# Performance work log

Measured on AMD Instinct MI355X. Metric: run time of the kernel, lower is better.

## Reference

```python
import jax, jax.numpy as jnp
import numpy as np

B, S, C, H = 2, 4096, 640, 8
D = C // H  # head_dim = 80


def setup_inputs() -> dict:
    key = jax.random.key(0)
    ks = jax.random.split(key, 5)
    init = 0.02
    return {
        "hidden_states": jax.random.normal(ks[0], (B, S, C), dtype=jnp.float32),
        "Wq": jax.random.normal(ks[1], (C, C), dtype=jnp.float32) * init,
        "Wk": jax.random.normal(ks[2], (C, C), dtype=jnp.float32) * init,
        "Wv": jax.random.normal(ks[3], (C, C), dtype=jnp.float32) * init,
        "Wo": jax.random.normal(ks[4], (C, C), dtype=jnp.float32) * init,
        "bo": jnp.zeros((C,), dtype=jnp.float32),
    }


def reference(hidden_states, Wq, Wk, Wv, Wo, bo):
    # self-attention: encoder_hidden_states is None -> k,v from hidden_states
    x = hidden_states  # [B, S, C]
    q = jnp.einsum("bsc,cd->bsd", x, Wq)
    k = jnp.einsum("bsc,cd->bsd", x, Wk)
    v = jnp.einsum("bsc,cd->bsd", x, Wv)

    # head_to_batch_dim: [B, S, H*D] -> [B, H, S, D]
    def split_heads(t):
        return t.reshape(B, S, H, D).transpose(0, 2, 1, 3)

    q, k, v = split_heads(q), split_heads(k), split_heads(v)

    scale = 1.0 / jnp.sqrt(jnp.float32(D))
    # get_attention_scores: baddbmm(q, k^T) * scale, softmax over keys
    scores = jnp.einsum("bhqd,bhkd->bhqk", q, k) * scale  # [B, H, S, S]
    probs = jax.nn.softmax(scores, axis=-1)
    out = jnp.einsum("bhqk,bhkd->bhqd", probs, v)  # [B, H, S, D]

    # batch_to_head_dim + to_out[0] linear (Dropout is identity at eval)
    out = out.transpose(0, 2, 1, 3).reshape(B, S, C)
    out = jnp.einsum("bsc,cd->bsd", out, Wo) + bo
    # residual_connection=False, rescale_output_factor=1.0 (diffusers defaults)
    return out
```

## Files before the change

kernel.cpp:

```cpp
#include <hip/hip_runtime.h>
#include <hip/hip_bf16.h>

typedef __bf16 bf16x8 __attribute__((ext_vector_type(8)));
typedef float f32x4 __attribute__((ext_vector_type(4)));
typedef float f32x16 __attribute__((ext_vector_type(16)));
typedef unsigned short u16;
typedef unsigned int u32;
typedef u16 u16x8 __attribute__((ext_vector_type(8)));

#define DEV __device__ __forceinline__

DEV u16 f2b(float f) {
    u32 u = __builtin_bit_cast(u32, f);
    u32 r = (u + 0x7FFFu + ((u >> 16) & 1u)) >> 16;
    return (u16)r;
}
DEV bf16x8 load8(const u16* p) {
    return __builtin_bit_cast(bf16x8, *(const uint4*)p);
}
DEV u32 cvtpk(float lo, float hi) {
    u32 r;
    asm("v_cvt_pk_bf16_f32 %0, %1, %2" : "=v"(r) : "v"(lo), "v"(hi));
    return r;
}
DEV void gld_lds16(const u16* g, const char* l) {
    __builtin_amdgcn_global_load_lds(
        (const __attribute__((address_space(1))) u32*)(unsigned long long)g,
        (__attribute__((address_space(3))) u32*)(u32)(unsigned long long)l,
        16, 0, 0);
}

__global__ __launch_bounds__(256) void cvt_x(const float* __restrict__ X, u16* __restrict__ Xb) {
    long i = ((long)blockIdx.x * 256 + threadIdx.x) * 8;
    float fa[8];
    *(uint4*)fa = *(const uint4*)(X + i);
    *(uint4*)(fa + 4) = *(const uint4*)(X + i + 4);
    u16x8 t;
    #pragma unroll
    for (int j = 0; j < 8; ++j) t[j] = f2b(fa[j]);
    *(u16x8*)(Xb + i) = t;
}

__global__ __launch_bounds__(256) void cvt_w4(
    const float* __restrict__ Wq, const float* __restrict__ Wk,
    const float* __restrict__ Wv, const float* __restrict__ Wo,
    u16* __restrict__ Wt4)
{
    const int z = blockIdx.z;
    const float* W = (z == 0) ? Wq : ((z == 1) ? Wk : ((z == 2) ? Wv : Wo));
    u16* Wt = Wt4 + (long)z * 409600;
    const int k0 = blockIdx.x * 64, n0 = blockIdx.y * 64;
    const int t = threadIdx.x;
    __shared__ u16 T[64][72];
    {
        int kl = t >> 2, nc = (t & 3) * 16;
        const float* src = W + (long)(k0 + kl) * 640 + n0 + nc;
        float fa[16];
        #pragma unroll
        for (int i = 0; i < 4; ++i) *(uint4*)(fa + i * 4) = *(const uint4*)(src + i * 4);
        #pragma unroll
        for (int j = 0; j < 16; ++j) T[nc + j][kl] = f2b(fa[j]);
    }
    __syncthreads();
    {
        int nl = t >> 2, kc = (t & 3) * 16;
        u16* dst = Wt + (long)(n0 + nl) * 640 + k0 + kc;
        *(uint4*)dst = *(const uint4*)&T[nl][kc];
        *(uint4*)(dst + 8) = *(const uint4*)&T[nl][kc + 8];
    }
}

#define GEMM_CORE(A_PTR, BT_PTR)                                                  \
    const int tid = threadIdx.x;                                                  \
    const int lane = tid & 63;                                                    \
    const int w = tid >> 6;                                                       \
    const int wm = w >> 1, wn = w & 1;                                            \
    const int lg = lane >> 4, lr = lane & 15;                                     \
    __shared__ __align__(16) char Bb[2][16384];                                   \
    auto stage = [&](int kt0, int buf) {                                          \
        _Pragma("unroll")                                                         \
        for (int i = 0; i < 4; ++i) {                                             \
            int c = i * 256 + tid;                                                \
            int n = c >> 3, cc = c & 7;                                           \
            gld_lds16(BT_PTR + (long)(n0 + n) * 640 + kt0 + ((cc ^ (n & 7)) * 8), \
                      Bb[buf] + (c & ~63) * 16);                                  \
        }                                                                         \
    };                                                                            \
    f32x4 acc[4][4] = {};                                                         \
    stage(0, 0);                                                                  \
    for (int t = 0; t < 10; ++t) {                                                \
        __syncthreads();                                                          \
        if (t < 9) stage((t + 1) * 64, (t + 1) & 1);                              \
        const char* Bc = Bb[t & 1];                                               \
        _Pragma("unroll")                                                         \
        for (int ks = 0; ks < 64; ks += 32) {                                     \
            bf16x8 a[4], b[4];                                                    \
            _Pragma("unroll")                                                     \
            for (int mi = 0; mi < 4; ++mi) {                                      \
                int row = m0 + wm * 64 + mi * 16 + lr;                            \
                a[mi] = load8(A_PTR + (long)row * 640 + t * 64 + ks + lg * 8);    \
            }                                                                     \
            _Pragma("unroll")                                                     \
            for (int ni = 0; ni < 4; ++ni) {                                      \
                int n = wn * 64 + ni * 16 + lr;                                   \
                int cc = (ks >> 3) + lg;                                          \
                b[ni] = __builtin_bit_cast(bf16x8,                                \
                    *(const uint4*)(Bc + (n * 8 + (cc ^ (n & 7))) * 16));         \
            }                                                                     \
            _Pragma("unroll")                                                     \
            for (int mi = 0; mi < 4; ++mi)                                        \
                _Pragma("unroll")                                                 \
                for (int ni = 0; ni < 4; ++ni)                                    \
                    acc[mi][ni] = __builtin_amdgcn_mfma_f32_16x16x32_bf16(        \
                        a[mi], b[ni], acc[mi][ni], 0, 0, 0);                      \
        }                                                                         \
    }

__global__ __launch_bounds__(256, 3) void gemm_qkv(
    const u16* __restrict__ X, const u16* __restrict__ Wt3,
    u16* __restrict__ q_ws, u16* __restrict__ k_ws, u16* __restrict__ v_ws)
{
    const int z = blockIdx.z;
    const u16* Wt = Wt3 + (long)z * 409600;
    const int m0 = blockIdx.x * 128;
    const int n0 = blockIdx.y * 128;
    GEMM_CORE(X, Wt)
    #pragma unroll
    for (int mi = 0; mi < 4; ++mi)
        #pragma unroll
        for (int ni = 0; ni < 4; ++ni)
            #pragma unroll
            for (int r = 0; r < 4; ++r) {
                int m = m0 + wm * 64 + mi * 16 + lg * 4 + r;
                int n = n0 + wn * 64 + ni * 16 + lr;
                int b_ = m >> 12, s = m & 4095;
                int h = n / 80, d = n % 80;
                long bh = b_ * 8 + h;
                int tt = s >> 6, jj = s & 63;
                float val = acc[mi][ni][r];
                if (z == 0) {
                    q_ws[(bh * 4096 + s) * 80 + d] = f2b(val * 0.16131517891624225f);
                } else if (z == 1) {
                    k_ws[(bh * 64 + tt) * 5120 + (((d >> 4) * 2 + ((d >> 3) & 1)) * 64 + jj) * 8 + (d & 7)] = f2b(val);
                } else {
                    int kb = jj >> 5, h2 = (jj >> 4) & 1, hv = (jj >> 2) & 1;
                    int jv = ((jj >> 3) & 1) * 4 + (jj & 3);
                    int c = kb * 2 + h2;
                    u16* vt = v_ws + (bh * 64 + tt) * 6144;
                    vt[((c * 2 + hv) * 96 + d) * 8 + jv] = f2b(val);
                    if (d == 0) vt[((c * 2 + hv) * 96 + 80) * 8 + jv] = 0x3F80;
                }
            }
}

__global__ __launch_bounds__(256, 3) void gemm_out(
    const u16* __restrict__ X, const u16* __restrict__ Wt,
    const float* __restrict__ bias, float* __restrict__ out)
{
    const int m0 = blockIdx.x * 128;
    const int n0 = blockIdx.y * 128;
    GEMM_CORE(X, Wt)
    #pragma unroll
    for (int mi = 0; mi < 4; ++mi)
        #pragma unroll
        for (int ni = 0; ni < 4; ++ni)
            #pragma unroll
            for (int r = 0; r < 4; ++r) {
                int m = m0 + wm * 64 + mi * 16 + lg * 4 + r;
                int n = n0 + wn * 64 + ni * 16 + lr;
                out[(long)m * 640 + n] = acc[mi][ni][r] + bias[n];
            }
}

__global__ __launch_bounds__(256, 2) void attn(
    const u16* __restrict__ q_ws, const u16* __restrict__ k_ws,
    const u16* __restrict__ v_ws, u16* __restrict__ o_ws)
{
    const int l = blockIdx.x;
    const int xcd = l & 7, inner = l >> 3;
    const int bh = (xcd << 1) | (inner >> 5);
    const int qx = inner & 31;
    const int qb = qx * 128;
    const int tid = threadIdx.x;
    const int lane = tid & 63;
    const int w = tid >> 6;
    const int hi = lane >> 5;
    const int lq = lane & 31;

    __shared__ __align__(16) char Kb[2][10240];
    __shared__ __align__(16) char Vb[2][12288];

    const u16* ktile = k_ws + (long)bh * 64 * 5120;
    const u16* vtile = v_ws + (long)bh * 64 * 6144;

    bf16x8 qf[5];
    const int qrow = qb + w * 32 + lq;
    #pragma unroll
    for (int kc = 0; kc < 5; ++kc)
        qf[kc] = load8(q_ws + ((long)bh * 4096 + qrow) * 80 + kc * 16 + hi * 8);

    f32x16 acc[3] = {};

    auto stage = [&](int t, int buf) {
        const u16* kt_ = ktile + (long)t * 5120;
        const u16* vt_ = vtile + (long)t * 6144;
        #pragma unroll
        for (int i = 0; i < 6; ++i) {
            int c = i * 256 + tid;
            if (c < 1408) {
                int cw = c & ~63;
                if (cw < 640) gld_lds16(kt_ + (long)c * 8, Kb[buf] + cw * 16);
                else          gld_lds16(vt_ + (long)(c - 640) * 8, Vb[buf] + (cw - 640) * 16);
            }
        }
    };

    stage(0, 0);
    for (int t = 0; t < 64; ++t) {
        __syncthreads();
        if (t < 63) stage(t + 1, (t + 1) & 1);
        const char* Kc = Kb[t & 1];
        const char* Vc = Vb[t & 1];

        f32x16 sf[2] = {};
        __builtin_amdgcn_s_setprio(1);
        #pragma unroll
        for (int kc = 0; kc < 5; ++kc) {
            #pragma unroll
            for (int kb = 0; kb < 2; ++kb) {
                bf16x8 kf = __builtin_bit_cast(bf16x8,
                    *(const uint4*)(Kc + ((kc * 2 + hi) * 64 + kb * 32 + lq) * 16));
                sf[kb] = __builtin_amdgcn_mfma_f32_32x32x16_bf16(kf, qf[kc], sf[kb], 0, 0, 0);
            }
        }
        __builtin_amdgcn_s_setprio(0);

        #pragma unroll
        for (int kb = 0; kb < 2; ++kb)
            #pragma unroll
            for (int r = 0; r < 16; ++r)
                sf[kb][r] = __builtin_amdgcn_exp2f(sf[kb][r]);

        bf16x8 pa[4];
        #pragma unroll
        for (int kb = 0; kb < 2; ++kb)
            #pragma unroll
            for (int h = 0; h < 2; ++h) {
                uint4 wv;
                wv.x = cvtpk(sf[kb][h * 8 + 0], sf[kb][h * 8 + 1]);
                wv.y = cvtpk(sf[kb][h * 8 + 2], sf[kb][h * 8 + 3]);
                wv.z = cvtpk(sf[kb][h * 8 + 4], sf[kb][h * 8 + 5]);
                wv.w = cvtpk(sf[kb][h * 8 + 6], sf[kb][h * 8 + 7]);
                pa[kb * 2 + h] = __builtin_bit_cast(bf16x8, wv);
            }

        __builtin_amdgcn_s_setprio(1);
        #pragma unroll
        for (int db = 0; db < 3; ++db)
            #pragma unroll
            for (int c = 0; c < 4; ++c) {
                bf16x8 vf = __builtin_bit_cast(bf16x8,
                    *(const uint4*)(Vc + ((c * 2 + hi) * 96 + db * 32 + lq) * 16));
                acc[db] = __builtin_amdgcn_mfma_f32_32x32x16_bf16(pa[c], vf, acc[db], 0, 0, 0);
            }
        __builtin_amdgcn_s_setprio(0);
    }

    const int b_ = bh >> 3, h8 = bh & 7;
    #pragma unroll
    for (int r = 0; r < 16; ++r) {
        int ql = (r & 3) + 8 * (r >> 2) + 4 * hi;
        float lsum = __shfl(acc[2][r], (hi << 5) + 16);
        float inv = 1.0f / lsum;
        int row = qb + w * 32 + ql;
        #pragma unroll
        for (int db = 0; db < 3; ++db) {
            int d = db * 32 + lq;
            if (d < 80)
                o_ws[((long)b_ * 4096 + row) * 640 + h8 * 80 + d] = f2b(acc[db][r] * inv);
        }
    }
}

extern "C" void kernel_launch(void* const* d_in, const int* in_sizes, int n_in,
                              void* d_out, int out_size, void* d_ws, size_t ws_size,
                              hipStream_t stream) {
    const float* x  = (const float*)d_in[0];
    const float* Wq = (const float*)d_in[1];
    const float* Wk = (const float*)d_in[2];
    const float* Wv = (const float*)d_in[3];
    const float* Wo = (const float*)d_in[4];
    const float* bo = (const float*)d_in[5];

    u16* ws = (u16*)d_ws;
    const long SZ = 5242880;
    u16* Xb   = ws;
    u16* q_ws = ws + SZ;
    u16* k_ws = ws + 2 * SZ;
    u16* v_ws = ws + 3 * SZ;
    u16* Wt4  = ws + 3 * SZ + 6291456;
    u16* o_ws = Xb;
    u16* WtO  = Wt4 + 3 * 409600;

    cvt_x<<<2560, 256, 0, stream>>>(x, Xb);
    dim3 gw4(10, 10, 4);
    cvt_w4<<<gw4, 256, 0, stream>>>(Wq, Wk, Wv, Wo, Wt4);

    dim3 g1(64, 5, 3);
    gemm_qkv<<<g1, 256, 0, stream>>>(Xb, Wt4, q_ws, k_ws, v_ws);

    attn<<<512, 256, 0, stream>>>(q_ws, k_ws, v_ws, o_ws);

    dim3 g3(64, 5);
    gemm_out<<<g3, 256, 0, stream>>>(o_ws, WtO, bo, (float*)d_out);
}
```

Measured before the change: 196.5 us.

## Software-pipeline attention QK with softmax/PV and merge conversion kernels

The attention loop is restructured so the QK^T MFMAs for the next key tile are issued before the exp/convert/PV work of the current tile, with V triple-buffered and K double-buffered in LDS. This is meant to overlap the exponential and conversion VALU work with matrix instructions and hide load latency. The two fp32-to-bf16 conversion kernels are also merged into one launch to save launch overhead. In exchange LDS use and register pressure go up, which could reduce occupancy. The clamped staging at the loop tail also issues redundant loads.

```diff
diff --git a/kernel.cpp b/kernel.cpp
--- a/kernel.cpp
+++ b/kernel.cpp
@@ -30,26 +30,30 @@
         16, 0, 0);
 }
 
-__global__ __launch_bounds__(256) void cvt_x(const float* __restrict__ X, u16* __restrict__ Xb) {
-    long i = ((long)blockIdx.x * 256 + threadIdx.x) * 8;
-    float fa[8];
-    *(uint4*)fa = *(const uint4*)(X + i);
-    *(uint4*)(fa + 4) = *(const uint4*)(X + i + 4);
-    u16x8 t;
-    #pragma unroll
-    for (int j = 0; j < 8; ++j) t[j] = f2b(fa[j]);
-    *(u16x8*)(Xb + i) = t;
-}
-
-__global__ __launch_bounds__(256) void cvt_w4(
+__global__ __launch_bounds__(256) void cvt_all(
+    const float* __restrict__ X, u16* __restrict__ Xb,
     const float* __restrict__ Wq, const float* __restrict__ Wk,
     const float* __restrict__ Wv, const float* __restrict__ Wo,
     u16* __restrict__ Wt4)
 {
-    const int z = blockIdx.z;
+    const int bx = blockIdx.x;
+    if (bx < 2560) {
+        long i = ((long)bx * 256 + threadIdx.x) * 8;
+        float fa[8];
+        *(uint4*)fa = *(const uint4*)(X + i);
+        *(uint4*)(fa + 4) = *(const uint4*)(X + i + 4);
+        u16x8 t;
+        #pragma unroll
+        for (int j = 0; j < 8; ++j) t[j] = f2b(fa[j]);
+        *(u16x8*)(Xb + i) = t;
+        return;
+    }
+    const int idx = bx - 2560;
+    const int z = idx / 100;
+    const int rem = idx % 100;
+    const int k0 = (rem / 10) * 64, n0 = (rem % 10) * 64;
     const float* W = (z == 0) ? Wq : ((z == 1) ? Wk : ((z == 2) ? Wv : Wo));
     u16* Wt = Wt4 + (long)z * 409600;
-    const int k0 = blockIdx.x * 64, n0 = blockIdx.y * 64;
     const int t = threadIdx.x;
     __shared__ u16 T[64][72];
     {
@@ -188,7 +192,7 @@
     const int lq = lane & 31;
 
     __shared__ __align__(16) char Kb[2][10240];
-    __shared__ __align__(16) char Vb[2][12288];
+    __shared__ __align__(16) char Vb[3][12288];
 
     const u16* ktile = k_ws + (long)bh * 64 * 5120;
     const u16* vtile = v_ws + (long)bh * 64 * 6144;
@@ -201,28 +205,26 @@
 
     f32x16 acc[3] = {};
 
-    auto stage = [&](int t, int buf) {
+    auto stageK = [&](int t, int buf) {
         const u16* kt_ = ktile + (long)t * 5120;
+        #pragma unroll
+        for (int i = 0; i < 3; ++i) {
+            int c = i * 256 + tid;
+            if (c < 640) gld_lds16(kt_ + (long)c * 8, Kb[buf] + (c & ~63) * 16);
+        }
+    };
+    auto stageV = [&](int t, int buf) {
         const u16* vt_ = vtile + (long)t * 6144;
         #pragma unroll
-        for (int i = 0; i < 6; ++i) {
+        for (int i = 0; i < 3; ++i) {
             int c = i * 256 + tid;
-            if (c < 1408) {
-                int cw = c & ~63;
-                if (cw < 640) gld_lds16(kt_ + (long)c * 8, Kb[buf] + cw * 16);
-                else          gld_lds16(vt_ + (long)(c - 640) * 8, Vb[buf] + (cw - 640) * 16);
-            }
+            gld_lds16(vt_ + (long)c * 8, Vb[buf] + (c & ~63) * 16);
         }
     };
-
-    stage(0, 0);
-    for (int t = 0; t < 64; ++t) {
-        __syncthreads();
-        if (t < 63) stage(t + 1, (t + 1) & 1);
-        const char* Kc = Kb[t & 1];
-        const char* Vc = Vb[t & 1];
-
-        f32x16 sf[2] = {};
+    auto QK = [&](int kbuf, f32x16* sf) {
+        const char* Kc = Kb[kbuf];
+        f32x16 z = {};
+        sf[0] = z; sf[1] = z;
         __builtin_amdgcn_s_setprio(1);
         #pragma unroll
         for (int kc = 0; kc < 5; ++kc) {
@@ -234,13 +236,14 @@
             }
         }
         __builtin_amdgcn_s_setprio(0);
-
+    };
+    auto SM_PV = [&](f32x16* sf, int vbuf) {
+        const char* Vc = Vb[vbuf];
         #pragma unroll
         for (int kb = 0; kb < 2; ++kb)
             #pragma unroll
             for (int r = 0; r < 16; ++r)
                 sf[kb][r] = __builtin_amdgcn_exp2f(sf[kb][r]);
-
         bf16x8 pa[4];
         #pragma unroll
         for (int kb = 0; kb < 2; ++kb)
@@ -253,7 +256,6 @@
                 wv.w = cvtpk(sf[kb][h * 8 + 6], sf[kb][h * 8 + 7]);
                 pa[kb * 2 + h] = __builtin_bit_cast(bf16x8, wv);
             }
-
         __builtin_amdgcn_s_setprio(1);
         #pragma unroll
         for (int db = 0; db < 3; ++db)
@@ -264,6 +266,31 @@
                 acc[db] = __builtin_amdgcn_mfma_f32_32x32x16_bf16(pa[c], vf, acc[db], 0, 0, 0);
             }
         __builtin_amdgcn_s_setprio(0);
+    };
+
+    f32x16 sfA[2], sfB[2];
+    stageK(0, 0); stageV(0, 0);
+    __syncthreads();
+    stageK(1, 1); stageV(1, 1);
+    QK(0, sfA);
+
+    for (int t = 0; t < 64; t += 2) {
+        __syncthreads();
+        {
+            int ts = (t + 2 < 64) ? t + 2 : 63;
+            stageK(ts, t & 1);
+            stageV(ts, (t + 2) % 3);
+        }
+        QK((t + 1) & 1, sfB);
+        SM_PV(sfA, t % 3);
+        __syncthreads();
+        {
+            int ts = (t + 3 < 64) ? t + 3 : 63;
+            stageK(ts, (t + 1) & 1);
+            stageV(ts, (t + 3) % 3);
+        }
+        QK(t & 1, sfA);
+        SM_PV(sfB, (t + 1) % 3);
     }
 
     const int b_ = bh >> 3, h8 = bh & 7;
@@ -302,9 +329,7 @@
     u16* o_ws = Xb;
     u16* WtO  = Wt4 + 3 * 409600;
 
-    cvt_x<<<2560, 256, 0, stream>>>(x, Xb);
-    dim3 gw4(10, 10, 4);
-    cvt_w4<<<gw4, 256, 0, stream>>>(Wq, Wk, Wv, Wo, Wt4);
+    cvt_all<<<2960, 256, 0, stream>>>(x, Xb, Wq, Wk, Wv, Wo, Wt4);
 
     dim3 g1(64, 5, 3);
     gemm_qkv<<<g1, 256, 0, stream>>>(Xb, Wt4, q_ws, k_ws, v_ws);
```

Measured after the change: 192.4 us. 2.1% less time.

## Split attention key tiles across wave pairs and merge conversion kernels

Applied to the files above, without the earlier changes.

The attention kernel now uses 64-row query blocks. Each pair of waves shares one 32-row query slice and splits every 64-key tile in half, so twice as many workgroups launch and occupancy hints go from 2 to 3 blocks per CU. At the end the partial output accumulators (row sums included) are added through shared memory, which costs an extra reduction, more K/V tile loads per query row, and more LDS use. Separately, the X and weight conversion kernels are fused into a single launch to drop one kernel launch.

```diff
diff --git a/kernel.cpp b/kernel.cpp
--- a/kernel.cpp
+++ b/kernel.cpp
@@ -30,26 +30,30 @@
         16, 0, 0);
 }
 
-__global__ __launch_bounds__(256) void cvt_x(const float* __restrict__ X, u16* __restrict__ Xb) {
-    long i = ((long)blockIdx.x * 256 + threadIdx.x) * 8;
-    float fa[8];
-    *(uint4*)fa = *(const uint4*)(X + i);
-    *(uint4*)(fa + 4) = *(const uint4*)(X + i + 4);
-    u16x8 t;
-    #pragma unroll
-    for (int j = 0; j < 8; ++j) t[j] = f2b(fa[j]);
-    *(u16x8*)(Xb + i) = t;
-}
-
-__global__ __launch_bounds__(256) void cvt_w4(
+__global__ __launch_bounds__(256) void cvt_all(
+    const float* __restrict__ X, u16* __restrict__ Xb,
     const float* __restrict__ Wq, const float* __restrict__ Wk,
     const float* __restrict__ Wv, const float* __restrict__ Wo,
     u16* __restrict__ Wt4)
 {
-    const int z = blockIdx.z;
+    const int bx = blockIdx.x;
+    if (bx < 2560) {
+        long i = ((long)bx * 256 + threadIdx.x) * 8;
+        float fa[8];
+        *(uint4*)fa = *(const uint4*)(X + i);
+        *(uint4*)(fa + 4) = *(const uint4*)(X + i + 4);
+        u16x8 t;
+        #pragma unroll
+        for (int j = 0; j < 8; ++j) t[j] = f2b(fa[j]);
+        *(u16x8*)(Xb + i) = t;
+        return;
+    }
+    const int idx = bx - 2560;
+    const int z = idx / 100;
+    const int rem = idx % 100;
+    const int k0 = (rem / 10) * 64, n0 = (rem % 10) * 64;
     const float* W = (z == 0) ? Wq : ((z == 1) ? Wk : ((z == 2) ? Wv : Wo));
     u16* Wt = Wt4 + (long)z * 409600;
-    const int k0 = blockIdx.x * 64, n0 = blockIdx.y * 64;
     const int t = threadIdx.x;
     __shared__ u16 T[64][72];
     {
@@ -172,29 +176,32 @@
             }
 }
 
-__global__ __launch_bounds__(256, 2) void attn(
+__global__ __launch_bounds__(256, 3) void attn(
     const u16* __restrict__ q_ws, const u16* __restrict__ k_ws,
     const u16* __restrict__ v_ws, u16* __restrict__ o_ws)
 {
     const int l = blockIdx.x;
     const int xcd = l & 7, inner = l >> 3;
-    const int bh = (xcd << 1) | (inner >> 5);
-    const int qx = inner & 31;
-    const int qb = qx * 128;
+    const int bh = (xcd << 1) | (inner >> 6);
+    const int qx = inner & 63;
+    const int qb = qx * 64;
     const int tid = threadIdx.x;
     const int lane = tid & 63;
     const int w = tid >> 6;
+    const int wq = w >> 1;
+    const int kb = w & 1;
     const int hi = lane >> 5;
     const int lq = lane & 31;
 
-    __shared__ __align__(16) char Kb[2][10240];
-    __shared__ __align__(16) char Vb[2][12288];
+    __shared__ __align__(16) char S[45056];
+    char* Kb = S;
+    char* Vb = S + 20480;
 
     const u16* ktile = k_ws + (long)bh * 64 * 5120;
     const u16* vtile = v_ws + (long)bh * 64 * 6144;
 
     bf16x8 qf[5];
-    const int qrow = qb + w * 32 + lq;
+    const int qrow = qb + wq * 32 + lq;
     #pragma unroll
     for (int kc = 0; kc < 5; ++kc)
         qf[kc] = load8(q_ws + ((long)bh * 4096 + qrow) * 80 + kc * 16 + hi * 8);
@@ -209,8 +216,8 @@
             int c = i * 256 + tid;
             if (c < 1408) {
                 int cw = c & ~63;
-                if (cw < 640) gld_lds16(kt_ + (long)c * 8, Kb[buf] + cw * 16);
-                else          gld_lds16(vt_ + (long)(c - 640) * 8, Vb[buf] + (cw - 640) * 16);
+                if (cw < 640) gld_lds16(kt_ + (long)c * 8, Kb + buf * 10240 + cw * 16);
+                else          gld_lds16(vt_ + (long)(c - 640) * 8, Vb + buf * 12288 + (cw - 640) * 16);
             }
         }
     };
@@ -219,65 +226,84 @@
     for (int t = 0; t < 64; ++t) {
         __syncthreads();
         if (t < 63) stage(t + 1, (t + 1) & 1);
-        const char* Kc = Kb[t & 1];
-        const char* Vc = Vb[t & 1];
-
-        f32x16 sf[2] = {};
+        const char* Kc = Kb + (t & 1) * 10240;
+        const char* Vc = Vb + (t & 1) * 12288;
+
+        f32x16 sf = {};
         __builtin_amdgcn_s_setprio(1);
         #pragma unroll
         for (int kc = 0; kc < 5; ++kc) {
-            #pragma unroll
-            for (int kb = 0; kb < 2; ++kb) {
-                bf16x8 kf = __builtin_bit_cast(bf16x8,
-                    *(const uint4*)(Kc + ((kc * 2 + hi) * 64 + kb * 32 + lq) * 16));
-                sf[kb] = __builtin_amdgcn_mfma_f32_32x32x16_bf16(kf, qf[kc], sf[kb], 0, 0, 0);
-            }
+            bf16x8 kf = __builtin_bit_cast(bf16x8,
+                *(const uint4*)(Kc + ((kc * 2 + hi) * 64 + kb * 32 + lq) * 16));
+            sf = __builtin_amdgcn_mfma_f32_32x32x16_bf16(kf, qf[kc], sf, 0, 0, 0);
         }
         __builtin_amdgcn_s_setprio(0);
 
         #pragma unroll
-        for (int kb = 0; kb < 2; ++kb)
-            #pragma unroll
-            for (int r = 0; r < 16; ++r)
-                sf[kb][r] = __builtin_amdgcn_exp2f(sf[kb][r]);
-
-        bf16x8 pa[4];
-        #pragma unroll
-        for (int kb = 0; kb < 2; ++kb)
+        for (int r = 0; r < 16; ++r)
+            sf[r] = __builtin_amdgcn_exp2f(sf[r]);
+
+        bf16x8 pa[2];
+        #pragma unroll
+        for (int h = 0; h < 2; ++h) {
+            uint4 wv;
+            wv.x = cvtpk(sf[h * 8 + 0], sf[h * 8 + 1]);
+            wv.y = cvtpk(sf[h * 8 + 2], sf[h * 8 + 3]);
+            wv.z = cvtpk(sf[h * 8 + 4], sf[h * 8 + 5]);
+            wv.w = cvtpk(sf[h * 8 + 6], sf[h * 8 + 7]);
+            pa[h] = __builtin_bit_cast(bf16x8, wv);
+        }
+
+        __builtin_amdgcn_s_setprio(1);
+        #pragma unroll
+        for (int db = 0; db < 3; ++db)
             #pragma unroll
             for (int h = 0; h < 2; ++h) {
-                uint4 wv;
-                wv.x = cvtpk(sf[kb][h * 8 + 0], sf[kb][h * 8 + 1]);
-                wv.y = cvtpk(sf[kb][h * 8 + 2], sf[kb][h * 8 + 3]);
-                wv.z = cvtpk(sf[kb][h * 8 + 4], sf[kb][h * 8 + 5]);
-                wv.w = cvtpk(sf[kb][h * 8 + 6], sf[kb][h * 8 + 7]);
-                pa[kb * 2 + h] = __builtin_bit_cast(bf16x8, wv);
-            }
-
-        __builtin_amdgcn_s_setprio(1);
+                bf16x8 vf = __builtin_bit_cast(bf16x8,
+                    *(const uint4*)(Vc + (((kb * 2 + h) * 2 + hi) * 96 + db * 32 + lq) * 16));
+                acc[db] = __builtin_amdgcn_mfma_f32_32x32x16_bf16(pa[h], vf, acc[db], 0, 0, 0);
+            }
+        __builtin_amdgcn_s_setprio(0);
+    }
+
+    __syncthreads();
+    float* comb = (float*)S;
+    const int crow = wq * 64 + lane;
+    if (kb == 1) {
         #pragma unroll
         for (int db = 0; db < 3; ++db)
             #pragma unroll
-            for (int c = 0; c < 4; ++c) {
-                bf16x8 vf = __builtin_bit_cast(bf16x8,
-                    *(const uint4*)(Vc + ((c * 2 + hi) * 96 + db * 32 + lq) * 16));
-                acc[db] = __builtin_amdgcn_mfma_f32_32x32x16_bf16(pa[c], vf, acc[db], 0, 0, 0);
-            }
-        __builtin_amdgcn_s_setprio(0);
-    }
-
-    const int b_ = bh >> 3, h8 = bh & 7;
-    #pragma unroll
-    for (int r = 0; r < 16; ++r) {
-        int ql = (r & 3) + 8 * (r >> 2) + 4 * hi;
-        float lsum = __shfl(acc[2][r], (hi << 5) + 16);
-        float inv = 1.0f / lsum;
-        int row = qb + w * 32 + ql;
-        #pragma unroll
-        for (int db = 0; db < 3; ++db) {
-            int d = db * 32 + lq;
-            if (d < 80)
-                o_ws[((long)b_ * 4096 + row) * 640 + h8 * 80 + d] = f2b(acc[db][r] * inv);
+            for (int j = 0; j < 4; ++j) {
+                f32x4 v4 = { acc[db][j * 4 + 0], acc[db][j * 4 + 1],
+                             acc[db][j * 4 + 2], acc[db][j * 4 + 3] };
+                *(f32x4*)(comb + crow * 48 + db * 16 + j * 4) = v4;
+            }
+    }
+    __syncthreads();
+    if (kb == 0) {
+        #pragma unroll
+        for (int db = 0; db < 3; ++db)
+            #pragma unroll
+            for (int j = 0; j < 4; ++j) {
+                f32x4 v4 = *(const f32x4*)(comb + crow * 48 + db * 16 + j * 4);
+                acc[db][j * 4 + 0] += v4[0];
+                acc[db][j * 4 + 1] += v4[1];
+                acc[db][j * 4 + 2] += v4[2];
+                acc[db][j * 4 + 3] += v4[3];
+            }
+        const int b_ = bh >> 3, h8 = bh & 7;
+        #pragma unroll
+        for (int r = 0; r < 16; ++r) {
+            int ql = (r & 3) + 8 * (r >> 2) + 4 * hi;
+            float lsum = __shfl(acc[2][r], (hi << 5) + 16);
+            float inv = 1.0f / lsum;
+            int row = qb + wq * 32 + ql;
+            #pragma unroll
+            for (int db = 0; db < 3; ++db) {
+                int d = db * 32 + lq;
+                if (d < 80)
+                    o_ws[((long)b_ * 4096 + row) * 640 + h8 * 80 + d] = f2b(acc[db][r] * inv);
+            }
         }
     }
 }
@@ -302,14 +328,12 @@
     u16* o_ws = Xb;
     u16* WtO  = Wt4 + 3 * 409600;
 
-    cvt_x<<<2560, 256, 0, stream>>>(x, Xb);
-    dim3 gw4(10, 10, 4);
-    cvt_w4<<<gw4, 256, 0, stream>>>(Wq, Wk, Wv, Wo, Wt4);
+    cvt_all<<<2960, 256, 0, stream>>>(x, Xb, Wq, Wk, Wv, Wo, Wt4);
 
     dim3 g1(64, 5, 3);
     gemm_qkv<<<g1, 256, 0, stream>>>(Xb, Wt4, q_ws, k_ws, v_ws);
 
-    attn<<<512, 256, 0, stream>>>(q_ws, k_ws, v_ws, o_ws);
+    attn<<<1024, 256, 0, stream>>>(q_ws, k_ws, v_ws, o_ws);
 
     dim3 g3(64, 5);
     gemm_out<<<g3, 256, 0, stream>>>(o_ws, WtO, bo, (float*)d_out);
```

Measured after the change: 219.8 us. 11.9% more time.

## Double query rows per wave in attention and merge conversion kernels

Applied to the files above, without the earlier changes.

Each attention wave now handles 64 query rows, split into two 32-row halves that share every K and V fragment read from LDS. This halves the grid to 256 blocks and drops the occupancy hint to 1 block per CU. The aim is to halve LDS fragment reads and global K/V staging per query row. The cost is roughly double the accumulator register pressure and fewer resident waves to hide latency. Separately, the X and weight conversion kernels are merged into one launch to save a kernel launch.

```diff
diff --git a/kernel.cpp b/kernel.cpp
--- a/kernel.cpp
+++ b/kernel.cpp
@@ -30,26 +30,30 @@
         16, 0, 0);
 }
 
-__global__ __launch_bounds__(256) void cvt_x(const float* __restrict__ X, u16* __restrict__ Xb) {
-    long i = ((long)blockIdx.x * 256 + threadIdx.x) * 8;
-    float fa[8];
-    *(uint4*)fa = *(const uint4*)(X + i);
-    *(uint4*)(fa + 4) = *(const uint4*)(X + i + 4);
-    u16x8 t;
-    #pragma unroll
-    for (int j = 0; j < 8; ++j) t[j] = f2b(fa[j]);
-    *(u16x8*)(Xb + i) = t;
-}
-
-__global__ __launch_bounds__(256) void cvt_w4(
+__global__ __launch_bounds__(256) void cvt_all(
+    const float* __restrict__ X, u16* __restrict__ Xb,
     const float* __restrict__ Wq, const float* __restrict__ Wk,
     const float* __restrict__ Wv, const float* __restrict__ Wo,
     u16* __restrict__ Wt4)
 {
-    const int z = blockIdx.z;
+    const int bx = blockIdx.x;
+    if (bx < 2560) {
+        long i = ((long)bx * 256 + threadIdx.x) * 8;
+        float fa[8];
+        *(uint4*)fa = *(const uint4*)(X + i);
+        *(uint4*)(fa + 4) = *(const uint4*)(X + i + 4);
+        u16x8 t;
+        #pragma unroll
+        for (int j = 0; j < 8; ++j) t[j] = f2b(fa[j]);
+        *(u16x8*)(Xb + i) = t;
+        return;
+    }
+    const int idx = bx - 2560;
+    const int z = idx / 100;
+    const int rem = idx % 100;
+    const int k0 = (rem / 10) * 64, n0 = (rem % 10) * 64;
     const float* W = (z == 0) ? Wq : ((z == 1) ? Wk : ((z == 2) ? Wv : Wo));
     u16* Wt = Wt4 + (long)z * 409600;
-    const int k0 = blockIdx.x * 64, n0 = blockIdx.y * 64;
     const int t = threadIdx.x;
     __shared__ u16 T[64][72];
     {
@@ -172,15 +176,15 @@
             }
 }
 
-__global__ __launch_bounds__(256, 2) void attn(
+__global__ __launch_bounds__(256, 1) void attn(
     const u16* __restrict__ q_ws, const u16* __restrict__ k_ws,
     const u16* __restrict__ v_ws, u16* __restrict__ o_ws)
 {
     const int l = blockIdx.x;
     const int xcd = l & 7, inner = l >> 3;
-    const int bh = (xcd << 1) | (inner >> 5);
-    const int qx = inner & 31;
-    const int qb = qx * 128;
+    const int bh = (xcd << 1) | (inner >> 4);
+    const int qx = inner & 15;
+    const int qb = qx * 256;
     const int tid = threadIdx.x;
     const int lane = tid & 63;
     const int w = tid >> 6;
@@ -193,13 +197,15 @@
     const u16* ktile = k_ws + (long)bh * 64 * 5120;
     const u16* vtile = v_ws + (long)bh * 64 * 6144;
 
-    bf16x8 qf[5];
-    const int qrow = qb + w * 32 + lq;
+    bf16x8 qfA[5], qfB[5];
+    const long qbase = ((long)bh * 4096 + qb + w * 64 + lq) * 80;
     #pragma unroll
-    for (int kc = 0; kc < 5; ++kc)
-        qf[kc] = load8(q_ws + ((long)bh * 4096 + qrow) * 80 + kc * 16 + hi * 8);
-
-    f32x16 acc[3] = {};
+    for (int kc = 0; kc < 5; ++kc) {
+        qfA[kc] = load8(q_ws + qbase + kc * 16 + hi * 8);
+        qfB[kc] = load8(q_ws + qbase + 32 * 80 + kc * 16 + hi * 8);
+    }
+
+    f32x16 accA[3] = {}, accB[3] = {};
 
     auto stage = [&](int t, int buf) {
         const u16* kt_ = ktile + (long)t * 5120;
@@ -222,37 +228,54 @@
         const char* Kc = Kb[t & 1];
         const char* Vc = Vb[t & 1];
 
-        f32x16 sf[2] = {};
+        f32x16 sfA0 = {}, sfA1 = {}, sfB0 = {}, sfB1 = {};
         __builtin_amdgcn_s_setprio(1);
         #pragma unroll
         for (int kc = 0; kc < 5; ++kc) {
-            #pragma unroll
-            for (int kb = 0; kb < 2; ++kb) {
-                bf16x8 kf = __builtin_bit_cast(bf16x8,
-                    *(const uint4*)(Kc + ((kc * 2 + hi) * 64 + kb * 32 + lq) * 16));
-                sf[kb] = __builtin_amdgcn_mfma_f32_32x32x16_bf16(kf, qf[kc], sf[kb], 0, 0, 0);
-            }
+            bf16x8 kf0 = __builtin_bit_cast(bf16x8,
+                *(const uint4*)(Kc + ((kc * 2 + hi) * 64 + lq) * 16));
+            bf16x8 kf1 = __builtin_bit_cast(bf16x8,
+                *(const uint4*)(Kc + ((kc * 2 + hi) * 64 + 32 + lq) * 16));
+            sfA0 = __builtin_amdgcn_mfma_f32_32x32x16_bf16(kf0, qfA[kc], sfA0, 0, 0, 0);
+            sfA1 = __builtin_amdgcn_mfma_f32_32x32x16_bf16(kf1, qfA[kc], sfA1, 0, 0, 0);
+            sfB0 = __builtin_amdgcn_mfma_f32_32x32x16_bf16(kf0, qfB[kc], sfB0, 0, 0, 0);
+            sfB1 = __builtin_amdgcn_mfma_f32_32x32x16_bf16(kf1, qfB[kc], sfB1, 0, 0, 0);
         }
         __builtin_amdgcn_s_setprio(0);
 
         #pragma unroll
-        for (int kb = 0; kb < 2; ++kb)
-            #pragma unroll
-            for (int r = 0; r < 16; ++r)
-                sf[kb][r] = __builtin_amdgcn_exp2f(sf[kb][r]);
-
-        bf16x8 pa[4];
-        #pragma unroll
-        for (int kb = 0; kb < 2; ++kb)
-            #pragma unroll
-            for (int h = 0; h < 2; ++h) {
-                uint4 wv;
-                wv.x = cvtpk(sf[kb][h * 8 + 0], sf[kb][h * 8 + 1]);
-                wv.y = cvtpk(sf[kb][h * 8 + 2], sf[kb][h * 8 + 3]);
-                wv.z = cvtpk(sf[kb][h * 8 + 4], sf[kb][h * 8 + 5]);
-                wv.w = cvtpk(sf[kb][h * 8 + 6], sf[kb][h * 8 + 7]);
-                pa[kb * 2 + h] = __builtin_bit_cast(bf16x8, wv);
-            }
+        for (int r = 0; r < 16; ++r) {
+            sfA0[r] = __builtin_amdgcn_exp2f(sfA0[r]);
+            sfA1[r] = __builtin_amdgcn_exp2f(sfA1[r]);
+            sfB0[r] = __builtin_amdgcn_exp2f(sfB0[r]);
+            sfB1[r] = __builtin_amdgcn_exp2f(sfB1[r]);
+        }
+
+        bf16x8 paA[4], paB[4];
+        #pragma unroll
+        for (int h = 0; h < 2; ++h) {
+            uint4 a0, a1, b0, b1;
+            a0.x = cvtpk(sfA0[h * 8 + 0], sfA0[h * 8 + 1]);
+            a0.y = cvtpk(sfA0[h * 8 + 2], sfA0[h * 8 + 3]);
+            a0.z = cvtpk(sfA0[h * 8 + 4], sfA0[h * 8 + 5]);
+            a0.w = cvtpk(sfA0[h * 8 + 6], sfA0[h * 8 + 7]);
+            paA[h] = __builtin_bit_cast(bf16x8, a0);
+            a1.x = cvtpk(sfA1[h * 8 + 0], sfA1[h * 8 + 1]);
+            a1.y = cvtpk(sfA1[h * 8 + 2], sfA1[h * 8 + 3]);
+            a1.z = cvtpk(sfA1[h * 8 + 4], sfA1[h * 8 + 5]);
+            a1.w = cvtpk(sfA1[h * 8 + 6], sfA1[h * 8 + 7]);
+            paA[2 + h] = __builtin_bit_cast(bf16x8, a1);
+            b0.x = cvtpk(sfB0[h * 8 + 0], sfB0[h * 8 + 1]);
+            b0.y = cvtpk(sfB0[h * 8 + 2], sfB0[h * 8 + 3]);
+            b0.z = cvtpk(sfB0[h * 8 + 4], sfB0[h * 8 + 5]);
+            b0.w = cvtpk(sfB0[h * 8 + 6], sfB0[h * 8 + 7]);
+            paB[h] = __builtin_bit_cast(bf16x8, b0);
+            b1.x = cvtpk(sfB1[h * 8 + 0], sfB1[h * 8 + 1]);
+            b1.y = cvtpk(sfB1[h * 8 + 2], sfB1[h * 8 + 3]);
+            b1.z = cvtpk(sfB1[h * 8 + 4], sfB1[h * 8 + 5]);
+            b1.w = cvtpk(sfB1[h * 8 + 6], sfB1[h * 8 + 7]);
+            paB[2 + h] = __builtin_bit_cast(bf16x8, b1);
+        }
 
         __builtin_amdgcn_s_setprio(1);
         #pragma unroll
@@ -261,7 +284,8 @@
             for (int c = 0; c < 4; ++c) {
                 bf16x8 vf = __builtin_bit_cast(bf16x8,
                     *(const uint4*)(Vc + ((c * 2 + hi) * 96 + db * 32 + lq) * 16));
-                acc[db] = __builtin_amdgcn_mfma_f32_32x32x16_bf16(pa[c], vf, acc[db], 0, 0, 0);
+                accA[db] = __builtin_amdgcn_mfma_f32_32x32x16_bf16(paA[c], vf, accA[db], 0, 0, 0);
+                accB[db] = __builtin_amdgcn_mfma_f32_32x32x16_bf16(paB[c], vf, accB[db], 0, 0, 0);
             }
         __builtin_amdgcn_s_setprio(0);
     }
@@ -270,14 +294,17 @@
     #pragma unroll
     for (int r = 0; r < 16; ++r) {
         int ql = (r & 3) + 8 * (r >> 2) + 4 * hi;
-        float lsum = __shfl(acc[2][r], (hi << 5) + 16);
-        float inv = 1.0f / lsum;
-        int row = qb + w * 32 + ql;
+        float invA = 1.0f / __shfl(accA[2][r], (hi << 5) + 16);
+        float invB = 1.0f / __shfl(accB[2][r], (hi << 5) + 16);
+        int rowA = qb + w * 64 + ql;
+        int rowB = rowA + 32;
         #pragma unroll
         for (int db = 0; db < 3; ++db) {
             int d = db * 32 + lq;
-            if (d < 80)
-                o_ws[((long)b_ * 4096 + row) * 640 + h8 * 80 + d] = f2b(acc[db][r] * inv);
+            if (d < 80) {
+                o_ws[((long)b_ * 4096 + rowA) * 640 + h8 * 80 + d] = f2b(accA[db][r] * invA);
+                o_ws[((long)b_ * 4096 + rowB) * 640 + h8 * 80 + d] = f2b(accB[db][r] * invB);
+            }
         }
     }
 }
@@ -302,14 +329,12 @@
     u16* o_ws = Xb;
     u16* WtO  = Wt4 + 3 * 409600;
 
-    cvt_x<<<2560, 256, 0, stream>>>(x, Xb);
-    dim3 gw4(10, 10, 4);
-    cvt_w4<<<gw4, 256, 0, stream>>>(Wq, Wk, Wv, Wo, Wt4);
+    cvt_all<<<2960, 256, 0, stream>>>(x, Xb, Wq, Wk, Wv, Wo, Wt4);
 
     dim3 g1(64, 5, 3);
     gemm_qkv<<<g1, 256, 0, stream>>>(Xb, Wt4, q_ws, k_ws, v_ws);
 
-    attn<<<512, 256, 0, stream>>>(q_ws, k_ws, v_ws, o_ws);
+    attn<<<256, 256, 0, stream>>>(q_ws, k_ws, v_ws, o_ws);
 
     dim3 g3(64, 5);
     gemm_out<<<g3, 256, 0, stream>>>(o_ws, WtO, bo, (float*)d_out);
```

Result: slower. 215.5 us (+9.7%).
